# Kernel tuning notes

Hardware: AMD Instinct MI355X
Metric: run time of the kernel (lower is better)

Reference implementation:

```python
import jax, jax.numpy as jnp
import numpy as np

HEIGHT = 450.0
# aspect_ratio = [input_h/450, input_w/450, 1] with input_shape=(224,224,3)
ASPECT = (224.0 / 450.0, 224.0 / 450.0, 1.0)

N_VERTS = 53215          # num_landmarks (full BFM mesh)
N_ROWS = 3 * N_VERTS     # 159645
EXP_DIM = 29
SHP_DIM = 199


def setup_inputs() -> dict:
    key = jax.random.key(0)
    ks = jax.random.split(key, 6)
    return {
        "pose_3DMM": jax.random.normal(ks[0], (1, 12), jnp.float32),
        "alpha_exp": jax.random.normal(ks[1], (1, EXP_DIM), jnp.float32),
        "alpha_shp": jax.random.normal(ks[2], (1, SHP_DIM), jnp.float32),
        "u_base": jax.random.normal(ks[3], (N_ROWS, 1), jnp.float32),
        "w_exp_base": jax.random.normal(ks[4], (N_ROWS, EXP_DIM), jnp.float32),
        "w_shp_base": jax.random.normal(ks[5], (N_ROWS, SHP_DIM), jnp.float32),
    }


def _transform_matrix(pose_3DMM, height):
    # pose_3DMM: (B, 12) -> (B, 3, 4); original code only supports B == 1
    Tm = pose_3DMM.reshape(-1, 3, 4)
    R = Tm[0, :, :3]                       # (3, 3)
    t_all = Tm[:, :, 3]                    # (B, 3)
    s = jnp.sum(t_all[-1])                 # scalar scale = sum of last translation (as in source)
    t = t_all[0] * jnp.array([1.0, 1.0, 0.0], Tm.dtype)  # zero out z (diag([1,1,0]) @ t)
    T = jnp.zeros((4, 4), Tm.dtype).at[:3, :3].set(R).at[3, 3].set(1.0)
    S = jnp.diag(jnp.concatenate([jnp.full((3,), s, Tm.dtype), jnp.ones((1,), Tm.dtype)]))
    T = S @ T
    M = jnp.eye(4, dtype=Tm.dtype).at[:3, 3].set(t)
    T = M @ T
    H = jnp.eye(4, dtype=Tm.dtype).at[1, 1].set(-1.0).at[1, 3].set(height)
    return H @ T                           # (4, 4)


def reference(pose_3DMM, alpha_exp, alpha_shp, u_base, w_exp_base, w_shp_base):
    # vertices: (B, 3N, 1) = u + W_exp @ a_exp + W_shp @ a_shp (broadcast batched matmul)
    vertices = u_base + (jnp.matmul(w_exp_base, alpha_exp[..., None])
                         + jnp.matmul(w_shp_base, alpha_shp[..., None]))
    B = vertices.shape[0]
    v = vertices.reshape(B, -1, 3)                        # (B, N, 3)
    T = _transform_matrix(pose_3DMM, jnp.asarray(HEIGHT, v.dtype))
    ones = jnp.ones((B, v.shape[1], 1), v.dtype)
    homo = jnp.concatenate([v, ones], axis=-1)            # (B, N, 4)
    img = jnp.matmul(homo, T.T)[:, :, :3]                 # (B, N, 3)
    return img * jnp.asarray(ASPECT, img.dtype)
```

## Files before the change

### kernel.cpp

```cpp
#include <hip/hip_runtime.h>

#define N_VERTS 53215
#define EXP_DIM 29
#define SHP_DIM 199
#define HEIGHT_F 450.0f
#define ASPECT_XY (224.0f / 450.0f)

__global__ __launch_bounds__(256, 8) void pca_transform_kernel(
    const float* __restrict__ pose,
    const float* __restrict__ alpha_exp,
    const float* __restrict__ alpha_shp,
    const float* __restrict__ u_base,
    const float* __restrict__ w_exp,
    const float* __restrict__ w_shp,
    float* __restrict__ out)
{
    const int lane   = threadIdx.x & 63;
    const int gwave  = (int)((blockIdx.x * blockDim.x + threadIdx.x) >> 6);
    const int nwaves = (int)((gridDim.x * blockDim.x) >> 6);

    const float p0 = pose[0], p1 = pose[1], p2  = pose[2],  p3  = pose[3];
    const float p4 = pose[4], p5 = pose[5], p6  = pose[6],  p7  = pose[7];
    const float p8 = pose[8], p9 = pose[9], p10 = pose[10], p11 = pose[11];
    const float s  = p3 + p7 + p11;

    const int  k3 = (lane < 7)  ? lane + 192 : 198;
    const int  ke = (lane < EXP_DIM) ? lane : (EXP_DIM - 1);
    const float a0 = alpha_shp[lane];
    const float a1 = alpha_shp[lane + 64];
    const float a2 = alpha_shp[lane + 128];
    const float a3 = (lane < 7) ? alpha_shp[k3] : 0.0f;
    const float ae = (lane < EXP_DIM) ? alpha_exp[ke] : 0.0f;

    for (int v = gwave; v < N_VERTS; v += nwaves) {
        const float* __restrict__ sx_p = w_shp + (size_t)(3 * v) * SHP_DIM;
        const float* __restrict__ sy_p = sx_p + SHP_DIM;
        const float* __restrict__ sz_p = sy_p + SHP_DIM;
        const float* __restrict__ ex_p = w_exp + (size_t)(3 * v) * EXP_DIM;

        const float x0 = sx_p[lane], x1 = sx_p[lane + 64], x2 = sx_p[lane + 128], x3 = sx_p[k3];
        const float y0 = sy_p[lane], y1 = sy_p[lane + 64], y2 = sy_p[lane + 128], y3 = sy_p[k3];
        const float z0 = sz_p[lane], z1 = sz_p[lane + 64], z2 = sz_p[lane + 128], z3 = sz_p[k3];
        const float xe = ex_p[ke], ye = ex_p[EXP_DIM + ke], ze = ex_p[2 * EXP_DIM + ke];
        const float ux = u_base[3 * v + 0];
        const float uy = u_base[3 * v + 1];
        const float uz = u_base[3 * v + 2];

        float sx = x0 * a0 + x1 * a1 + x2 * a2 + x3 * a3 + xe * ae;
        float sy = y0 * a0 + y1 * a1 + y2 * a2 + y3 * a3 + ye * ae;
        float sz = z0 * a0 + z1 * a1 + z2 * a2 + z3 * a3 + ze * ae;

        #pragma unroll
        for (int off = 32; off > 0; off >>= 1) {
            sx += __shfl_xor(sx, off, 64);
            sy += __shfl_xor(sy, off, 64);
            sz += __shfl_xor(sz, off, 64);
        }

        const float vx = sx + ux;
        const float vy = sy + uy;
        const float vz = sz + uz;

        const float ox = ASPECT_XY * (s * (p0 * vx + p1 * vy + p2  * vz) + p3);
        const float oy = ASPECT_XY * (HEIGHT_F - (s * (p4 * vx + p5 * vy + p6 * vz) + p7));
        const float oz = s * (p8 * vx + p9 * vy + p10 * vz);

        if (lane == 0) {
            float* o = out + (size_t)v * 3;
            o[0] = ox; o[1] = oy; o[2] = oz;
        }
    }
}

extern "C" void kernel_launch(void* const* d_in, const int* in_sizes, int n_in,
                              void* d_out, int out_size, void* d_ws, size_t ws_size,
                              hipStream_t stream) {
    const float* pose      = (const float*)d_in[0];
    const float* alpha_exp = (const float*)d_in[1];
    const float* alpha_shp = (const float*)d_in[2];
    const float* u_base    = (const float*)d_in[3];
    const float* w_exp     = (const float*)d_in[4];
    const float* w_shp     = (const float*)d_in[5];
    float* out = (float*)d_out;

    pca_transform_kernel<<<2048, 256, 0, stream>>>(
        pose, alpha_exp, alpha_shp, u_base, w_exp, w_shp, out);
}
```

Measured before the change: 205.5 us.

## Process two vertices per wave with DPP reductions and vectorized stores

Result: no change. 204.4 us (-0.6%).

```diff
diff --git a/kernel.cpp b/kernel.cpp
--- a/kernel.cpp
+++ b/kernel.cpp
@@ -6,7 +6,17 @@
 #define HEIGHT_F 450.0f
 #define ASPECT_XY (224.0f / 450.0f)
 
-__global__ __launch_bounds__(256, 8) void pca_transform_kernel(
+#define DPP_ADD_STEP(s, ctrl)                                                  \
+  s += __int_as_float(__builtin_amdgcn_update_dpp(                             \
+      0, __float_as_int(s), (ctrl), 0xf, 0xf, true))
+
+#define WAVE_REDUCE_6(s0, s1, s2, s3, s4, s5, ctrl)                            \
+  do {                                                                         \
+    DPP_ADD_STEP(s0, ctrl); DPP_ADD_STEP(s1, ctrl); DPP_ADD_STEP(s2, ctrl);    \
+    DPP_ADD_STEP(s3, ctrl); DPP_ADD_STEP(s4, ctrl); DPP_ADD_STEP(s5, ctrl);    \
+  } while (0)
+
+__global__ __launch_bounds__(256, 4) void pca_transform_kernel(
     const float* __restrict__ pose,
     const float* __restrict__ alpha_exp,
     const float* __restrict__ alpha_shp,
@@ -15,8 +25,9 @@
     const float* __restrict__ w_shp,
     float* __restrict__ out)
 {
-    const int lane   = threadIdx.x & 63;
-    const int gwave  = (int)((blockIdx.x * blockDim.x + threadIdx.x) >> 6);
+    const int lane = threadIdx.x & 63;
+    const int gwave =
+        __builtin_amdgcn_readfirstlane((int)((blockIdx.x * blockDim.x + threadIdx.x) >> 6));
     const int nwaves = (int)((gridDim.x * blockDim.x) >> 6);
 
     const float p0 = pose[0], p1 = pose[1], p2  = pose[2],  p3  = pose[3];
@@ -32,42 +43,70 @@
     const float a3 = (lane < 7) ? alpha_shp[k3] : 0.0f;
     const float ae = (lane < EXP_DIM) ? alpha_exp[ke] : 0.0f;
 
-    for (int v = gwave; v < N_VERTS; v += nwaves) {
-        const float* __restrict__ sx_p = w_shp + (size_t)(3 * v) * SHP_DIM;
-        const float* __restrict__ sy_p = sx_p + SHP_DIM;
-        const float* __restrict__ sz_p = sy_p + SHP_DIM;
-        const float* __restrict__ ex_p = w_exp + (size_t)(3 * v) * EXP_DIM;
+    const int ngroups = (N_VERTS + 1) >> 1;
+    for (int g = gwave; g < ngroups; g += nwaves) {
+        const int v0 = g << 1;
+        const int v1 = (v0 + 1 < N_VERTS) ? v0 + 1 : v0;
 
-        const float x0 = sx_p[lane], x1 = sx_p[lane + 64], x2 = sx_p[lane + 128], x3 = sx_p[k3];
-        const float y0 = sy_p[lane], y1 = sy_p[lane + 64], y2 = sy_p[lane + 128], y3 = sy_p[k3];
-        const float z0 = sz_p[lane], z1 = sz_p[lane + 64], z2 = sz_p[lane + 128], z3 = sz_p[k3];
-        const float xe = ex_p[ke], ye = ex_p[EXP_DIM + ke], ze = ex_p[2 * EXP_DIM + ke];
-        const float ux = u_base[3 * v + 0];
-        const float uy = u_base[3 * v + 1];
-        const float uz = u_base[3 * v + 2];
+        const float* __restrict__ A  = w_shp + (size_t)(3 * v0) * SHP_DIM;
+        const float* __restrict__ B  = w_shp + (size_t)(3 * v1) * SHP_DIM;
+        const float* __restrict__ EA = w_exp + (size_t)(3 * v0) * EXP_DIM;
+        const float* __restrict__ EB = w_exp + (size_t)(3 * v1) * EXP_DIM;
 
-        float sx = x0 * a0 + x1 * a1 + x2 * a2 + x3 * a3 + xe * ae;
-        float sy = y0 * a0 + y1 * a1 + y2 * a2 + y3 * a3 + ye * ae;
-        float sz = z0 * a0 + z1 * a1 + z2 * a2 + z3 * a3 + ze * ae;
+        const float ax0 = A[lane],               ax1 = A[lane + 64];
+        const float ax2 = A[lane + 128],         ax3 = A[k3];
+        const float ay0 = A[SHP_DIM + lane],     ay1 = A[SHP_DIM + lane + 64];
+        const float ay2 = A[SHP_DIM + lane + 128], ay3 = A[SHP_DIM + k3];
+        const float az0 = A[2*SHP_DIM + lane],   az1 = A[2*SHP_DIM + lane + 64];
+        const float az2 = A[2*SHP_DIM + lane + 128], az3 = A[2*SHP_DIM + k3];
+        const float bx0 = B[lane],               bx1 = B[lane + 64];
+        const float bx2 = B[lane + 128],         bx3 = B[k3];
+        const float by0 = B[SHP_DIM + lane],     by1 = B[SHP_DIM + lane + 64];
+        const float by2 = B[SHP_DIM + lane + 128], by3 = B[SHP_DIM + k3];
+        const float bz0 = B[2*SHP_DIM + lane],   bz1 = B[2*SHP_DIM + lane + 64];
+        const float bz2 = B[2*SHP_DIM + lane + 128], bz3 = B[2*SHP_DIM + k3];
+        const float aex = EA[ke], aey = EA[EXP_DIM + ke], aez = EA[2*EXP_DIM + ke];
+        const float bex = EB[ke], bey = EB[EXP_DIM + ke], bez = EB[2*EXP_DIM + ke];
+        const float ux0 = u_base[3 * v0 + 0];
+        const float uy0 = u_base[3 * v0 + 1];
+        const float uz0 = u_base[3 * v0 + 2];
+        const float ux1 = u_base[3 * v1 + 0];
+        const float uy1 = u_base[3 * v1 + 1];
+        const float uz1 = u_base[3 * v1 + 2];
 
-        #pragma unroll
-        for (int off = 32; off > 0; off >>= 1) {
-            sx += __shfl_xor(sx, off, 64);
-            sy += __shfl_xor(sy, off, 64);
-            sz += __shfl_xor(sz, off, 64);
-        }
+        float sx0 = ax0*a0 + ax1*a1 + ax2*a2 + ax3*a3 + aex*ae;
+        float sy0 = ay0*a0 + ay1*a1 + ay2*a2 + ay3*a3 + aey*ae;
+        float sz0 = az0*a0 + az1*a1 + az2*a2 + az3*a3 + aez*ae;
+        float sx1 = bx0*a0 + bx1*a1 + bx2*a2 + bx3*a3 + bex*ae;
+        float sy1 = by0*a0 + by1*a1 + by2*a2 + by3*a3 + bey*ae;
+        float sz1 = bz0*a0 + bz1*a1 + bz2*a2 + bz3*a3 + bez*ae;
 
-        const float vx = sx + ux;
-        const float vy = sy + uy;
-        const float vz = sz + uz;
+        WAVE_REDUCE_6(sx0, sy0, sz0, sx1, sy1, sz1, 0x111);
+        WAVE_REDUCE_6(sx0, sy0, sz0, sx1, sy1, sz1, 0x112);
+        WAVE_REDUCE_6(sx0, sy0, sz0, sx1, sy1, sz1, 0x114);
+        WAVE_REDUCE_6(sx0, sy0, sz0, sx1, sy1, sz1, 0x118);
+        WAVE_REDUCE_6(sx0, sy0, sz0, sx1, sy1, sz1, 0x142);
+        WAVE_REDUCE_6(sx0, sy0, sz0, sx1, sy1, sz1, 0x143);
 
-        const float ox = ASPECT_XY * (s * (p0 * vx + p1 * vy + p2  * vz) + p3);
-        const float oy = ASPECT_XY * (HEIGHT_F - (s * (p4 * vx + p5 * vy + p6 * vz) + p7));
-        const float oz = s * (p8 * vx + p9 * vy + p10 * vz);
+        const float vx0 = sx0 + ux0, vy0 = sy0 + uy0, vz0 = sz0 + uz0;
+        const float vx1 = sx1 + ux1, vy1 = sy1 + uy1, vz1 = sz1 + uz1;
 
-        if (lane == 0) {
-            float* o = out + (size_t)v * 3;
-            o[0] = ox; o[1] = oy; o[2] = oz;
+        const float ox0 = ASPECT_XY * (s * (p0*vx0 + p1*vy0 + p2 *vz0) + p3);
+        const float oy0 = ASPECT_XY * (HEIGHT_F - (s * (p4*vx0 + p5*vy0 + p6*vz0) + p7));
+        const float oz0 = s * (p8*vx0 + p9*vy0 + p10*vz0);
+        const float ox1 = ASPECT_XY * (s * (p0*vx1 + p1*vy1 + p2 *vz1) + p3);
+        const float oy1 = ASPECT_XY * (HEIGHT_F - (s * (p4*vx1 + p5*vy1 + p6*vz1) + p7));
+        const float oz1 = s * (p8*vx1 + p9*vy1 + p10*vz1);
+
+        if (lane == 63) {
+            float* o = out + (size_t)3 * v0;
+            if (v1 != v0) {
+                *reinterpret_cast<float2*>(o)     = make_float2(ox0, oy0);
+                *reinterpret_cast<float2*>(o + 2) = make_float2(oz0, ox1);
+                *reinterpret_cast<float2*>(o + 4) = make_float2(oy1, oz1);
+            } else {
+                o[0] = ox0; o[1] = oy0; o[2] = oz0;
+            }
         }
     }
 }
```

## Vectorize per-vertex row loads with float4 and reduce with DPP instead of shuffles

Applied to the files above, without the earlier changes.

New measurement: 209.4 us. No clear change (+1.9%).

```diff
diff --git a/kernel.cpp b/kernel.cpp
--- a/kernel.cpp
+++ b/kernel.cpp
@@ -6,7 +6,22 @@
 #define HEIGHT_F 450.0f
 #define ASPECT_XY (224.0f / 450.0f)
 
-__global__ __launch_bounds__(256, 8) void pca_transform_kernel(
+typedef float f4 __attribute__((ext_vector_type(4)));
+
+#define DPP_ADD_STEP(s, ctrl)                                                  \
+  s += __int_as_float(__builtin_amdgcn_update_dpp(                             \
+      0, __float_as_int(s), (ctrl), 0xf, 0xf, true))
+
+#define WAVE_REDUCE_3(s0, s1, s2, ctrl)                                        \
+  do {                                                                         \
+    DPP_ADD_STEP(s0, ctrl); DPP_ADD_STEP(s1, ctrl); DPP_ADD_STEP(s2, ctrl);    \
+  } while (0)
+
+__device__ __forceinline__ float dot4(f4 a, f4 b) {
+    return a.x * b.x + a.y * b.y + a.z * b.z + a.w * b.w;
+}
+
+__global__ __launch_bounds__(256, 4) void pca_transform_kernel(
     const float* __restrict__ pose,
     const float* __restrict__ alpha_exp,
     const float* __restrict__ alpha_shp,
@@ -15,8 +30,9 @@
     const float* __restrict__ w_shp,
     float* __restrict__ out)
 {
-    const int lane   = threadIdx.x & 63;
-    const int gwave  = (int)((blockIdx.x * blockDim.x + threadIdx.x) >> 6);
+    const int lane = threadIdx.x & 63;
+    const int gwave =
+        __builtin_amdgcn_readfirstlane((int)((blockIdx.x * blockDim.x + threadIdx.x) >> 6));
     const int nwaves = (int)((gridDim.x * blockDim.x) >> 6);
 
     const float p0 = pose[0], p1 = pose[1], p2  = pose[2],  p3  = pose[3];
@@ -24,48 +40,66 @@
     const float p8 = pose[8], p9 = pose[9], p10 = pose[10], p11 = pose[11];
     const float s  = p3 + p7 + p11;
 
-    const int  k3 = (lane < 7)  ? lane + 192 : 198;
-    const int  ke = (lane < EXP_DIM) ? lane : (EXP_DIM - 1);
-    const float a0 = alpha_shp[lane];
-    const float a1 = alpha_shp[lane + 64];
-    const float a2 = alpha_shp[lane + 128];
-    const float a3 = (lane < 7) ? alpha_shp[k3] : 0.0f;
+    const int   ke = (lane < EXP_DIM) ? lane : (EXP_DIM - 1);
     const float ae = (lane < EXP_DIM) ? alpha_exp[ke] : 0.0f;
 
+    f4 W0x, W0y, W1y, W1z, W2z;
+    {
+        const int b = 4 * lane;
+        #pragma unroll
+        for (int e = 0; e < 4; ++e) {
+            const int j0 = b + e;
+            const int j1 = 256 + b + e;
+            const int j2 = 512 + b + e;
+            const float w0 = alpha_shp[(j0 < SHP_DIM) ? j0 : (j0 - SHP_DIM)];
+            W0x[e] = (j0 < SHP_DIM) ? w0 : 0.0f;
+            W0y[e] = (j0 < SHP_DIM) ? 0.0f : w0;
+            const float w1 = alpha_shp[(j1 < 2 * SHP_DIM) ? (j1 - SHP_DIM)
+                                                          : (j1 - 2 * SHP_DIM)];
+            W1y[e] = (j1 < 2 * SHP_DIM) ? w1 : 0.0f;
+            W1z[e] = (j1 < 2 * SHP_DIM) ? 0.0f : w1;
+            W2z[e] = (j2 <= 595) ? alpha_shp[j2 - 2 * SHP_DIM] : 0.0f;
+        }
+    }
+    const float w596 = (lane == 0) ? alpha_shp[SHP_DIM - 1] : 0.0f;
+    const int   l2   = (lane < 21) ? lane : 0;
+
     for (int v = gwave; v < N_VERTS; v += nwaves) {
-        const float* __restrict__ sx_p = w_shp + (size_t)(3 * v) * SHP_DIM;
-        const float* __restrict__ sy_p = sx_p + SHP_DIM;
-        const float* __restrict__ sz_p = sy_p + SHP_DIM;
-        const float* __restrict__ ex_p = w_exp + (size_t)(3 * v) * EXP_DIM;
+        const float* __restrict__ p = w_shp + (size_t)v * (3 * SHP_DIM);
+        const float* __restrict__ e = w_exp + (size_t)v * (3 * EXP_DIM);
 
-        const float x0 = sx_p[lane], x1 = sx_p[lane + 64], x2 = sx_p[lane + 128], x3 = sx_p[k3];
-        const float y0 = sy_p[lane], y1 = sy_p[lane + 64], y2 = sy_p[lane + 128], y3 = sy_p[k3];
-        const float z0 = sz_p[lane], z1 = sz_p[lane + 64], z2 = sz_p[lane + 128], z3 = sz_p[k3];
-        const float xe = ex_p[ke], ye = ex_p[EXP_DIM + ke], ze = ex_p[2 * EXP_DIM + ke];
+        const f4 q0 = *(const f4*)(p + 4 * lane);
+        const f4 q1 = *(const f4*)(p + 256 + 4 * lane);
+        const f4 q2 = *(const f4*)(p + 512 + 4 * l2);
+        const float t596 = p[596];
+        const float exv = e[ke];
+        const float eyv = e[EXP_DIM + ke];
+        const float ezv = e[2 * EXP_DIM + ke];
         const float ux = u_base[3 * v + 0];
         const float uy = u_base[3 * v + 1];
         const float uz = u_base[3 * v + 2];
 
-        float sx = x0 * a0 + x1 * a1 + x2 * a2 + x3 * a3 + xe * ae;
-        float sy = y0 * a0 + y1 * a1 + y2 * a2 + y3 * a3 + ye * ae;
-        float sz = z0 * a0 + z1 * a1 + z2 * a2 + z3 * a3 + ze * ae;
+        float sx = dot4(q0, W0x);
+        float sy = dot4(q0, W0y) + dot4(q1, W1y);
+        float sz = dot4(q1, W1z) + dot4(q2, W2z) + t596 * w596;
+        sx += exv * ae;
+        sy += eyv * ae;
+        sz += ezv * ae;
 
-        #pragma unroll
-        for (int off = 32; off > 0; off >>= 1) {
-            sx += __shfl_xor(sx, off, 64);
-            sy += __shfl_xor(sy, off, 64);
-            sz += __shfl_xor(sz, off, 64);
-        }
+        WAVE_REDUCE_3(sx, sy, sz, 0x111);
+        WAVE_REDUCE_3(sx, sy, sz, 0x112);
+        WAVE_REDUCE_3(sx, sy, sz, 0x114);
+        WAVE_REDUCE_3(sx, sy, sz, 0x118);
+        WAVE_REDUCE_3(sx, sy, sz, 0x142);
+        WAVE_REDUCE_3(sx, sy, sz, 0x143);
 
-        const float vx = sx + ux;
-        const float vy = sy + uy;
-        const float vz = sz + uz;
+        const float vx = sx + ux, vy = sy + uy, vz = sz + uz;
 
         const float ox = ASPECT_XY * (s * (p0 * vx + p1 * vy + p2  * vz) + p3);
         const float oy = ASPECT_XY * (HEIGHT_F - (s * (p4 * vx + p5 * vy + p6 * vz) + p7));
         const float oz = s * (p8 * vx + p9 * vy + p10 * vz);
 
-        if (lane == 0) {
+        if (lane == 63) {
             float* o = out + (size_t)v * 3;
             o[0] = ox; o[1] = oy; o[2] = oz;
         }
```
